# Kernel tuning notes

Hardware: AMD Instinct MI355X
Metric: run time of the kernel (lower is better)

## Reference

```python
import jax, jax.numpy as jnp
import numpy as np

HIDDEN = 2048
N_HEADS = 32
N_KV_HEADS = 8
HEAD_DIM = 64
MAX_SEQ_LEN = 512
ROPE_BASE = 10000.0


def _rope_tables(seq_len):
    inv_freq = 1.0 / (ROPE_BASE ** (jnp.arange(0, HEAD_DIM, 2, dtype=jnp.float32) / HEAD_DIM))
    pos = jnp.arange(seq_len, dtype=jnp.float32)
    freqs = jnp.outer(pos, inv_freq)              # [S, D/2]
    emb = jnp.concatenate([freqs, freqs], axis=-1)  # [S, D]
    return jnp.cos(emb), jnp.sin(emb)


def _rotate_half(x):
    h = x.shape[-1] // 2
    return jnp.concatenate([-x[..., h:], x[..., :h]], axis=-1)


def _apply_rope(x, cos, sin):
    # x: [B, H, S, D]; cos/sin: [S, D] broadcast over batch/heads
    return x * cos[None, None] + _rotate_half(x) * sin[None, None]


def setup_inputs() -> dict:
    key = jax.random.key(0)
    ks = jax.random.split(key, 5)
    B, S = 8, 512
    x = jax.random.normal(ks[0], (B, S, HIDDEN), dtype=jnp.float32)
    sq = 0.02
    Wq = jax.random.normal(ks[1], (HIDDEN, N_HEADS * HEAD_DIM), dtype=jnp.float32) * sq
    Wk = jax.random.normal(ks[2], (HIDDEN, N_KV_HEADS * HEAD_DIM), dtype=jnp.float32) * sq
    Wv = jax.random.normal(ks[3], (HIDDEN, N_KV_HEADS * HEAD_DIM), dtype=jnp.float32) * sq
    Wo = jax.random.normal(ks[4], (N_HEADS * HEAD_DIM, HIDDEN), dtype=jnp.float32) * sq
    return {"x": x, "Wq": Wq, "Wk": Wk, "Wv": Wv, "Wo": Wo}


def reference(x, Wq, Wk, Wv, Wo):
    B, S, _ = x.shape
    groups = N_HEADS // N_KV_HEADS
    scale = HEAD_DIM ** -0.5

    q = (x @ Wq).reshape(B, S, N_HEADS, HEAD_DIM).transpose(0, 2, 1, 3)      # [B,H,S,D]
    k = (x @ Wk).reshape(B, S, N_KV_HEADS, HEAD_DIM).transpose(0, 2, 1, 3)   # [B,Hk,S,D]
    v = (x @ Wv).reshape(B, S, N_KV_HEADS, HEAD_DIM).transpose(0, 2, 1, 3)

    cos, sin = _rope_tables(S)
    q = _apply_rope(q, cos, sin)
    k = _apply_rope(k, cos, sin)

    kv_cache = (k, v)  # returned before GQA head duplication, as in the original

    # repeat_interleave over kv heads for GQA
    kr = jnp.repeat(k, groups, axis=1)  # [B,H,S,D]
    vr = jnp.repeat(v, groups, axis=1)

    scores = jnp.einsum("bhqd,bhkd->bhqk", q, kr) * scale  # [B,H,S,S]
    causal = jnp.triu(jnp.ones((S, S), dtype=bool), k=1)
    scores = jnp.where(causal[None, None], -jnp.inf, scores)
    probs = jax.nn.softmax(scores, axis=-1)
    out = jnp.einsum("bhqk,bhkd->bhqd", probs, vr)  # [B,H,S,D]
    out = out.transpose(0, 2, 1, 3).reshape(B, S, N_HEADS * HEAD_DIM)
    out = out @ Wo
    return (out, kv_cache[0], kv_cache[1])
```

## Files before the change

kernel.cpp:

```cpp
#include <hip/hip_runtime.h>
#include <math.h>

#define BATCH   8
#define SEQ     512
#define HID     2048
#define NH      32
#define NKV     8
#define HD      64

typedef unsigned short u16;
typedef __attribute__((ext_vector_type(8))) short  s16x8;
typedef __attribute__((ext_vector_type(4))) float  f32x4;

__device__ __forceinline__ u16 f2bf(float f) {
  unsigned u = __builtin_bit_cast(unsigned, f);
  u += 0x7fffu + ((u >> 16) & 1u);
  return (u16)(u >> 16);
}
__device__ __forceinline__ float bf2f(u16 h) {
  unsigned u = ((unsigned)h) << 16;
  return __builtin_bit_cast(float, u);
}
__device__ __forceinline__ void split_bf16(float v, u16& h, u16& l) {
  h = f2bf(v);
  l = f2bf(v - bf2f(h));
}

#define GL16(gp, lp) __builtin_amdgcn_global_load_lds(                         \
    (const __attribute__((address_space(1))) void*)(gp),                       \
    (__attribute__((address_space(3))) void*)(lp), 16, 0, 0)

#define MFMA16(a, b, c) __builtin_amdgcn_mfma_f32_16x16x32_bf16((a), (b), (c), 0, 0, 0)

__global__ __launch_bounds__(256) void cast_x(const float* __restrict__ src,
                                              u16* __restrict__ dst)
{
  int i = blockIdx.x * 256 + threadIdx.x;
  float4 v = ((const float4*)src)[i];
  ushort4 hh;
  hh.x = f2bf(v.x); hh.y = f2bf(v.y); hh.z = f2bf(v.z); hh.w = f2bf(v.w);
  ((ushort4*)dst)[i] = hh;
}

__global__ __launch_bounds__(256) void tsplit_w(const float* __restrict__ W, int N,
                                                u16* __restrict__ BTh,
                                                u16* __restrict__ BTl, int nofs)
{
  __shared__ float t[64][68];
  const int nt = blockIdx.x * 64, kt = blockIdx.y * 64;
  const int tid = threadIdx.x;
  const int c4 = (tid & 15) * 4, r0 = tid >> 4;
  #pragma unroll
  for (int i = 0; i < 4; i++) {
    int r = r0 + i * 16;
    float4 v = *(const float4*)(&W[(size_t)(kt + r) * N + nt + c4]);
    t[c4 + 0][r] = v.x; t[c4 + 1][r] = v.y; t[c4 + 2][r] = v.z; t[c4 + 3][r] = v.w;
  }
  __syncthreads();
  #pragma unroll
  for (int i = 0; i < 4; i++) {
    int rr = r0 + i * 16;
    float4 v = *(const float4*)(&t[rr][c4]);
    ushort4 hh, ll;
    split_bf16(v.x, hh.x, ll.x);
    split_bf16(v.y, hh.y, ll.y);
    split_bf16(v.z, hh.z, ll.z);
    split_bf16(v.w, hh.w, ll.w);
    size_t o = (size_t)(nofs + nt + rr) * 2048 + kt + c4;
    *(ushort4*)(&BTh[o]) = hh;
    *(ushort4*)(&BTl[o]) = ll;
  }
}

__device__ __forceinline__ void gemm_main2(
    const u16* __restrict__ A,
    const u16* __restrict__ Bh, const u16* __restrict__ Bl,
    int mtile, int ntile,
    u16* sA, u16* sBh, u16* sBl,
    f32x4 acc[4][4])
{
  const int tid  = threadIdx.x;
  const int lane = tid & 63;
  const int w    = tid >> 6;
  const int wr = (w >> 1) * 64, wc = (w & 1) * 64;
  const int fr = lane & 15, fk = (lane >> 4) * 8;

  const int r0 = tid >> 2, c0 = (tid & 3) * 8;
  const size_t a0 = (size_t)(mtile + r0) * 2048 + c0;
  const size_t a1 = (size_t)(mtile + r0 + 64) * 2048 + c0;
  const size_t b0 = (size_t)(ntile + r0) * 2048 + c0;
  const size_t b1 = (size_t)(ntile + r0 + 64) * 2048 + c0;
  const int d0 = tid * 8, d1 = tid * 8 + 2048;

  for (int kt = 0; kt < 2048; kt += 32) {
    GL16(A  + a0 + kt, sA  + d0);
    GL16(A  + a1 + kt, sA  + d1);
    GL16(Bh + b0 + kt, sBh + d0);
    GL16(Bh + b1 + kt, sBh + d1);
    GL16(Bl + b0 + kt, sBl + d0);
    GL16(Bl + b1 + kt, sBl + d1);
    __syncthreads();

    s16x8 bhf[4], blf[4];
    #pragma unroll
    for (int ni = 0; ni < 4; ni++) {
      bhf[ni] = *(const s16x8*)(&sBh[(wc + ni * 16 + fr) * 32 + fk]);
      blf[ni] = *(const s16x8*)(&sBl[(wc + ni * 16 + fr) * 32 + fk]);
    }
    #pragma unroll
    for (int mi = 0; mi < 4; mi++) {
      s16x8 a = *(const s16x8*)(&sA[(wr + mi * 16 + fr) * 32 + fk]);
      #pragma unroll
      for (int ni = 0; ni < 4; ni++) {
        f32x4 c = acc[mi][ni];
        c = MFMA16(a, bhf[ni], c);
        c = MFMA16(a, blf[ni], c);
        acc[mi][ni] = c;
      }
    }
    __syncthreads();
  }
}

__device__ __forceinline__ void gemm_main1(
    const u16* __restrict__ A, const u16* __restrict__ B,
    int mtile, int ntile,
    u16* sA, u16* sB,
    f32x4 acc[4][4])
{
  const int tid  = threadIdx.x;
  const int lane = tid & 63;
  const int w    = tid >> 6;
  const int wr = (w >> 1) * 64, wc = (w & 1) * 64;
  const int fr = lane & 15, fk = (lane >> 4) * 8;

  const int r0 = tid >> 2, c0 = (tid & 3) * 8;
  const size_t a0 = (size_t)(mtile + r0) * 2048 + c0;
  const size_t a1 = (size_t)(mtile + r0 + 64) * 2048 + c0;
  const size_t b0 = (size_t)(ntile + r0) * 2048 + c0;
  const size_t b1 = (size_t)(ntile + r0 + 64) * 2048 + c0;
  const int d0 = tid * 8, d1 = tid * 8 + 2048;

  for (int kt = 0; kt < 2048; kt += 32) {
    GL16(A + a0 + kt, sA + d0);
    GL16(A + a1 + kt, sA + d1);
    GL16(B + b0 + kt, sB + d0);
    GL16(B + b1 + kt, sB + d1);
    __syncthreads();

    s16x8 bf[4];
    #pragma unroll
    for (int ni = 0; ni < 4; ni++)
      bf[ni] = *(const s16x8*)(&sB[(wc + ni * 16 + fr) * 32 + fk]);
    #pragma unroll
    for (int mi = 0; mi < 4; mi++) {
      s16x8 a = *(const s16x8*)(&sA[(wr + mi * 16 + fr) * 32 + fk]);
      #pragma unroll
      for (int ni = 0; ni < 4; ni++)
        acc[mi][ni] = MFMA16(a, bf[ni], acc[mi][ni]);
    }
    __syncthreads();
  }
}

#define L2_10K 13.28771238f

__global__ __launch_bounds__(256, 2) void gemm_qkv(
    const u16* __restrict__ A,
    const u16* __restrict__ Bh, const u16* __restrict__ Bl,
    u16* __restrict__ Qh, u16* __restrict__ Ql,
    float* __restrict__ kout, float* __restrict__ vout,
    u16* __restrict__ Kh, u16* __restrict__ Kl, u16* __restrict__ Vt)
{
  __shared__ __align__(16) u16 sA[128 * 32], sBh[128 * 32], sBl[128 * 32];
  const int ntile = blockIdx.x * 128, mtile = blockIdx.y * 128;
  f32x4 acc[4][4] = {};
  gemm_main2(A, Bh, Bl, mtile, ntile, sA, sBh, sBl, acc);

  const int lane = threadIdx.x & 63, w = threadIdx.x >> 6;
  const int wr = (w >> 1) * 64, wc = (w & 1) * 64;
  const int orow = (lane >> 4) * 4, ocol = lane & 15;

  if (ntile < 2048) {
    float inv[2];
    #pragma unroll
    for (int nj = 0; nj < 2; nj++)
      inv[nj] = exp2f((float)(nj * 16 + ocol) * (-L2_10K / 32.0f));
    #pragma unroll
    for (int mi = 0; mi < 4; mi++)
      #pragma unroll
      for (int r = 0; r < 4; r++) {
        int m = mtile + wr + mi * 16 + orow + r;
        int s = m & 511;
        #pragma unroll
        for (int nj = 0; nj < 2; nj++) {
          float th = (float)s * inv[nj];
          float sn, cs; sincosf(th, &sn, &cs);
          float a0 = acc[mi][nj][r]     * 0.125f;
          float a1 = acc[mi][nj + 2][r] * 0.125f;
          float q0 = a0 * cs - a1 * sn;
          float q1 = a1 * cs + a0 * sn;
          size_t o0 = (size_t)m * 2048 + ntile + wc + nj * 16 + ocol;
          u16 hh, ll;
          split_bf16(q0, hh, ll); Qh[o0] = hh;      Ql[o0] = ll;
          split_bf16(q1, hh, ll); Qh[o0 + 32] = hh; Ql[o0 + 32] = ll;
        }
      }
  } else if (ntile < 2560) {
    float inv[2];
    #pragma unroll
    for (int nj = 0; nj < 2; nj++)
      inv[nj] = exp2f((float)(nj * 16 + ocol) * (-L2_10K / 32.0f));
    #pragma unroll
    for (int mi = 0; mi < 4; mi++)
      #pragma unroll
      for (int r = 0; r < 4; r++) {
        int m = mtile + wr + mi * 16 + orow + r;
        int bb = m >> 9, s = m & 511;
        #pragma unroll
        for (int nj = 0; nj < 2; nj++) {
          int np = ntile + wc + nj * 16 + ocol - 2048;
          int hk = np >> 6, d = np & 63;
          float th = (float)s * inv[nj];
          float sn, cs; sincosf(th, &sn, &cs);
          float a0 = acc[mi][nj][r];
          float a1 = acc[mi][nj + 2][r];
          float k0 = a0 * cs - a1 * sn;
          float k1 = a1 * cs + a0 * sn;
          size_t o = ((size_t)(bb * 8 + hk) * 512 + s) * 64 + d;
          kout[o] = k0; kout[o + 32] = k1;
          u16 hh, ll;
          split_bf16(k0, hh, ll); Kh[o] = hh;      Kl[o] = ll;
          split_bf16(k1, hh, ll); Kh[o + 32] = hh; Kl[o + 32] = ll;
        }
      }
  } else {
    #pragma unroll
    for (int mi = 0; mi < 4; mi++)
      #pragma unroll
      for (int ni = 0; ni < 4; ni++) {
        int np = ntile + wc + ni * 16 + ocol - 2560;
        int hk = np >> 6, d = np & 63;
        int m0 = mtile + wr + mi * 16 + orow;
        int bb = m0 >> 9, s0 = m0 & 511;
        ushort4 pk;
        #pragma unroll
        for (int r = 0; r < 4; r++) {
          float v = acc[mi][ni][r];
          vout[((size_t)(bb * 8 + hk) * 512 + s0 + r) * 64 + d] = v;
          ((u16*)&pk)[r] = f2bf(v);
        }
        *(ushort4*)(&Vt[((size_t)(bb * 8 + hk) * 64 + d) * 512 + s0]) = pk;
      }
  }
}

__global__ __launch_bounds__(256, 2) void gemm_out(
    const u16* __restrict__ A, const u16* __restrict__ B,
    float* __restrict__ Cout)
{
  __shared__ __align__(16) u16 sA[128 * 32], sB[128 * 32];
  const int ntile = blockIdx.x * 128, mtile = blockIdx.y * 128;
  f32x4 acc[4][4] = {};
  gemm_main1(A, B, mtile, ntile, sA, sB, acc);

  const int lane = threadIdx.x & 63, w = threadIdx.x >> 6;
  const int wr = (w >> 1) * 64, wc = (w & 1) * 64;
  const int orow = (lane >> 4) * 4, ocol = lane & 15;
  #pragma unroll
  for (int mi = 0; mi < 4; mi++)
    #pragma unroll
    for (int r = 0; r < 4; r++) {
      int m = mtile + wr + mi * 16 + orow + r;
      #pragma unroll
      for (int ni = 0; ni < 4; ni++)
        Cout[(size_t)m * 2048 + ntile + wc + ni * 16 + ocol] = acc[mi][ni][r];
    }
}

__global__ __launch_bounds__(256, 2)
void attn(const u16* __restrict__ Qh, const u16* __restrict__ Ql,
          const u16* __restrict__ Kh, const u16* __restrict__ Kl,
          const u16* __restrict__ Vt,
          u16* __restrict__ Ao)
{
  __shared__ __align__(16) u16 sKh[4096], sKl[4096], sVt[4096];
  __shared__ __align__(16) u16 sP[4][1024];

  const int qt = blockIdx.x, h = blockIdx.y, bb = blockIdx.z;
  const int hk = h >> 2, bh = bb * 8 + hk;
  const int tid = threadIdx.x, lane = tid & 63, w = tid >> 6;
  const int fr = lane & 15, fg = lane >> 4;

  const int qrow = bb * 512 + qt * 64 + w * 16 + fr;
  const size_t qoff = (size_t)qrow * 2048 + h * 64 + fg * 8;
  const s16x8 qh0 = *(const s16x8*)(Qh + qoff);
  const s16x8 qh1 = *(const s16x8*)(Qh + qoff + 32);
  const s16x8 ql0 = *(const s16x8*)(Ql + qoff);
  const s16x8 ql1 = *(const s16x8*)(Ql + qoff + 32);

  f32x4 oacc[4] = {};
  float m_r[4] = {-1e30f, -1e30f, -1e30f, -1e30f};
  float l_r[4] = {};

  const size_t kbase = (size_t)bh * 512 * 64;
  const size_t vbase = (size_t)bh * 64 * 512;

  for (int j = 0; j <= qt; j++) {
    __syncthreads();
    #pragma unroll
    for (int p = 0; p < 2; p++) {
      int s = tid + p * 256;
      int row = s >> 3, c8 = (s & 7) ^ (row & 7);
      GL16(Kh + kbase + (size_t)(j * 64 + row) * 64 + c8 * 8, sKh + s * 8);
      GL16(Kl + kbase + (size_t)(j * 64 + row) * 64 + c8 * 8, sKl + s * 8);
      GL16(Vt + vbase + (size_t)row * 512 + j * 64 + c8 * 8,  sVt + s * 8);
    }
    __syncthreads();

    f32x4 sacc[4] = {};
    #pragma unroll
    for (int ni = 0; ni < 4; ni++) {
      #pragma unroll
      for (int ks = 0; ks < 2; ks++) {
        int row = ni * 16 + fr;
        int byte = row * 128 + ((fg * 16 + ks * 64) ^ ((row & 7) << 4));
        s16x8 kh = *(const s16x8*)((const char*)sKh + byte);
        s16x8 kl = *(const s16x8*)((const char*)sKl + byte);
        s16x8 qa = ks ? qh1 : qh0;
        s16x8 qb = ks ? ql1 : ql0;
        f32x4 c = sacc[ni];
        c = MFMA16(qa, kh, c);
        c = MFMA16(qa, kl, c);
        c = MFMA16(qb, kh, c);
        sacc[ni] = c;
      }
    }

    const int rowg0 = qt * 64 + w * 16 + fg * 4;
    #pragma unroll
    for (int r = 0; r < 4; r++) {
      float mx = -1e30f;
      #pragma unroll
      for (int ni = 0; ni < 4; ni++) {
        int col = j * 64 + ni * 16 + fr;
        float v = (col <= rowg0 + r) ? sacc[ni][r] : -1e30f;
        sacc[ni][r] = v;
        mx = fmaxf(mx, v);
      }
      mx = fmaxf(mx, __shfl_xor(mx, 1));
      mx = fmaxf(mx, __shfl_xor(mx, 2));
      mx = fmaxf(mx, __shfl_xor(mx, 4));
      mx = fmaxf(mx, __shfl_xor(mx, 8));
      float mnew = fmaxf(m_r[r], mx);
      float sc = __expf(m_r[r] - mnew);
      m_r[r] = mnew;
      float ls = 0.0f;
      #pragma unroll
      for (int ni = 0; ni < 4; ni++) {
        float p = __expf(sacc[ni][r] - mnew);
        sacc[ni][r] = p;
        ls += p;
      }
      ls += __shfl_xor(ls, 1);
      ls += __shfl_xor(ls, 2);
      ls += __shfl_xor(ls, 4);
      ls += __shfl_xor(ls, 8);
      l_r[r] = l_r[r] * sc + ls;
      #pragma unroll
      for (int nd = 0; nd < 4; nd++) oacc[nd][r] *= sc;
    }

    u16* pbuf = sP[w];
    #pragma unroll
    for (int ni = 0; ni < 4; ni++)
      #pragma unroll
      for (int r = 0; r < 4; r++) {
        int prow = fg * 4 + r, pcol = ni * 16 + fr;
        int byte = prow * 128 + ((pcol * 2) ^ ((prow & 7) << 4));
        *(u16*)((char*)pbuf + byte) = f2bf(sacc[ni][r]);
      }

    #pragma unroll
    for (int ks = 0; ks < 2; ks++) {
      int pbyte = fr * 128 + ((fg * 16 + ks * 64) ^ ((fr & 7) << 4));
      s16x8 pa = *(const s16x8*)((const char*)pbuf + pbyte);
      #pragma unroll
      for (int nd = 0; nd < 4; nd++) {
        int vrow = nd * 16 + fr;
        int vbyte = vrow * 128 + ((fg * 16 + ks * 64) ^ ((vrow & 7) << 4));
        s16x8 vb = *(const s16x8*)((const char*)sVt + vbyte);
        oacc[nd] = MFMA16(pa, vb, oacc[nd]);
      }
    }
  }

  const size_t obase = (size_t)(bb * 512 + qt * 64 + w * 16 + fg * 4) * 2048 + h * 64;
  #pragma unroll
  for (int r = 0; r < 4; r++) {
    float inv = 1.0f / l_r[r];
    #pragma unroll
    for (int nd = 0; nd < 4; nd++)
      Ao[obase + (size_t)r * 2048 + nd * 16 + fr] = f2bf(oacc[nd][r] * inv);
  }
}

extern "C" void kernel_launch(void* const* d_in, const int* in_sizes, int n_in,
                              void* d_out, int out_size, void* d_ws, size_t ws_size,
                              hipStream_t stream)
{
  const float* x  = (const float*)d_in[0];
  const float* Wq = (const float*)d_in[1];
  const float* Wk = (const float*)d_in[2];
  const float* Wv = (const float*)d_in[3];
  const float* Wo = (const float*)d_in[4];

  float* out  = (float*)d_out;
  float* kout = out + 8388608;
  float* vout = out + 10485760;

  uint8_t* wsb = (uint8_t*)d_ws;
  u16* xbf = (u16*)(wsb + 0);
  u16* Ao  = xbf;
  u16* Wqh = (u16*)(wsb + 16777216);
  u16* Wql = (u16*)(wsb + 29360128);
  u16* Woh = (u16*)(wsb + 16777216);
  u16* Wol = (u16*)(wsb + 25165824);
  u16* Qhp = (u16*)(wsb + 41943040);
  u16* Qlp = (u16*)(wsb + 58720256);
  u16* Khp = (u16*)(wsb + 75497472);
  u16* Klp = (u16*)(wsb + 79691776);
  u16* Vtp = (u16*)(wsb + 83886080);

  cast_x<<<8192, 256, 0, stream>>>(x, xbf);
  tsplit_w<<<dim3(32, 32), 256, 0, stream>>>(Wq, 2048, Wqh, Wql, 0);
  tsplit_w<<<dim3(8, 32), 256, 0, stream>>>(Wk, 512, Wqh, Wql, 2048);
  tsplit_w<<<dim3(8, 32), 256, 0, stream>>>(Wv, 512, Wqh, Wql, 2560);
  gemm_qkv<<<dim3(24, 32), 256, 0, stream>>>(xbf, Wqh, Wql,
                                             Qhp, Qlp, kout, vout, Khp, Klp, Vtp);
  tsplit_w<<<dim3(32, 32), 256, 0, stream>>>(Wo, 2048, Woh, Wol, 0);
  attn<<<dim3(8, 32, 8), 256, 0, stream>>>(Qhp, Qlp, Khp, Klp, Vtp, Ao);
  gemm_out<<<dim3(16, 32), 256, 0, stream>>>(Ao, Woh, out);
}
```

Measured before the change: 359.0 us.

## Drop split-bf16 weight and K terms, read K/V directly from global in attention

Weights and K are now cast to a single bf16 instead of being split into high and low bf16 halves. This halves the MFMA count and the B-operand traffic in the QKV GEMM, and drops one MFMA per K fragment in attention. The attention kernel no longer stages K and V through LDS. Each wave loads its fragments straight from global memory with no block barriers, and the occupancy hint is raised to 4 blocks per CU. This trades accuracy, since the weight and K low parts are lost, and gives up LDS reuse of K/V across the 4 waves in exchange for less sync and more occupancy.

```diff
diff --git a/kernel.cpp b/kernel.cpp
--- a/kernel.cpp
+++ b/kernel.cpp
@@ -42,9 +42,8 @@
   ((ushort4*)dst)[i] = hh;
 }
 
-__global__ __launch_bounds__(256) void tsplit_w(const float* __restrict__ W, int N,
-                                                u16* __restrict__ BTh,
-                                                u16* __restrict__ BTl, int nofs)
+__global__ __launch_bounds__(256) void tcast_w(const float* __restrict__ W, int N,
+                                               u16* __restrict__ BT, int nofs)
 {
   __shared__ float t[64][68];
   const int nt = blockIdx.x * 64, kt = blockIdx.y * 64;
@@ -61,22 +60,16 @@
   for (int i = 0; i < 4; i++) {
     int rr = r0 + i * 16;
     float4 v = *(const float4*)(&t[rr][c4]);
-    ushort4 hh, ll;
-    split_bf16(v.x, hh.x, ll.x);
-    split_bf16(v.y, hh.y, ll.y);
-    split_bf16(v.z, hh.z, ll.z);
-    split_bf16(v.w, hh.w, ll.w);
-    size_t o = (size_t)(nofs + nt + rr) * 2048 + kt + c4;
-    *(ushort4*)(&BTh[o]) = hh;
-    *(ushort4*)(&BTl[o]) = ll;
-  }
-}
-
-__device__ __forceinline__ void gemm_main2(
-    const u16* __restrict__ A,
-    const u16* __restrict__ Bh, const u16* __restrict__ Bl,
+    ushort4 hh;
+    hh.x = f2bf(v.x); hh.y = f2bf(v.y); hh.z = f2bf(v.z); hh.w = f2bf(v.w);
+    *(ushort4*)(&BT[(size_t)(nofs + nt + rr) * 2048 + kt + c4]) = hh;
+  }
+}
+
+__device__ __forceinline__ void gemm_main1(
+    const u16* __restrict__ A, const u16* __restrict__ B,
     int mtile, int ntile,
-    u16* sA, u16* sBh, u16* sBl,
+    u16* sA, u16* sB,
     f32x4 acc[4][4])
 {
   const int tid  = threadIdx.x;
@@ -93,55 +86,6 @@
   const int d0 = tid * 8, d1 = tid * 8 + 2048;
 
   for (int kt = 0; kt < 2048; kt += 32) {
-    GL16(A  + a0 + kt, sA  + d0);
-    GL16(A  + a1 + kt, sA  + d1);
-    GL16(Bh + b0 + kt, sBh + d0);
-    GL16(Bh + b1 + kt, sBh + d1);
-    GL16(Bl + b0 + kt, sBl + d0);
-    GL16(Bl + b1 + kt, sBl + d1);
-    __syncthreads();
-
-    s16x8 bhf[4], blf[4];
-    #pragma unroll
-    for (int ni = 0; ni < 4; ni++) {
-      bhf[ni] = *(const s16x8*)(&sBh[(wc + ni * 16 + fr) * 32 + fk]);
-      blf[ni] = *(const s16x8*)(&sBl[(wc + ni * 16 + fr) * 32 + fk]);
-    }
-    #pragma unroll
-    for (int mi = 0; mi < 4; mi++) {
-      s16x8 a = *(const s16x8*)(&sA[(wr + mi * 16 + fr) * 32 + fk]);
-      #pragma unroll
-      for (int ni = 0; ni < 4; ni++) {
-        f32x4 c = acc[mi][ni];
-        c = MFMA16(a, bhf[ni], c);
-        c = MFMA16(a, blf[ni], c);
-        acc[mi][ni] = c;
-      }
-    }
-    __syncthreads();
-  }
-}
-
-__device__ __forceinline__ void gemm_main1(
-    const u16* __restrict__ A, const u16* __restrict__ B,
-    int mtile, int ntile,
-    u16* sA, u16* sB,
-    f32x4 acc[4][4])
-{
-  const int tid  = threadIdx.x;
-  const int lane = tid & 63;
-  const int w    = tid >> 6;
-  const int wr = (w >> 1) * 64, wc = (w & 1) * 64;
-  const int fr = lane & 15, fk = (lane >> 4) * 8;
-
-  const int r0 = tid >> 2, c0 = (tid & 3) * 8;
-  const size_t a0 = (size_t)(mtile + r0) * 2048 + c0;
-  const size_t a1 = (size_t)(mtile + r0 + 64) * 2048 + c0;
-  const size_t b0 = (size_t)(ntile + r0) * 2048 + c0;
-  const size_t b1 = (size_t)(ntile + r0 + 64) * 2048 + c0;
-  const int d0 = tid * 8, d1 = tid * 8 + 2048;
-
-  for (int kt = 0; kt < 2048; kt += 32) {
     GL16(A + a0 + kt, sA + d0);
     GL16(A + a1 + kt, sA + d1);
     GL16(B + b0 + kt, sB + d0);
@@ -166,16 +110,15 @@
 #define L2_10K 13.28771238f
 
 __global__ __launch_bounds__(256, 2) void gemm_qkv(
-    const u16* __restrict__ A,
-    const u16* __restrict__ Bh, const u16* __restrict__ Bl,
+    const u16* __restrict__ A, const u16* __restrict__ B,
     u16* __restrict__ Qh, u16* __restrict__ Ql,
     float* __restrict__ kout, float* __restrict__ vout,
-    u16* __restrict__ Kh, u16* __restrict__ Kl, u16* __restrict__ Vt)
-{
-  __shared__ __align__(16) u16 sA[128 * 32], sBh[128 * 32], sBl[128 * 32];
+    u16* __restrict__ Kp, u16* __restrict__ Vt)
+{
+  __shared__ __align__(16) u16 sA[128 * 32], sB[128 * 32];
   const int ntile = blockIdx.x * 128, mtile = blockIdx.y * 128;
   f32x4 acc[4][4] = {};
-  gemm_main2(A, Bh, Bl, mtile, ntile, sA, sBh, sBl, acc);
+  gemm_main1(A, B, mtile, ntile, sA, sB, acc);
 
   const int lane = threadIdx.x & 63, w = threadIdx.x >> 6;
   const int wr = (w >> 1) * 64, wc = (w & 1) * 64;
@@ -228,10 +171,8 @@
           float k0 = a0 * cs - a1 * sn;
           float k1 = a1 * cs + a0 * sn;
           size_t o = ((size_t)(bb * 8 + hk) * 512 + s) * 64 + d;
-          kout[o] = k0; kout[o + 32] = k1;
-          u16 hh, ll;
-          split_bf16(k0, hh, ll); Kh[o] = hh;      Kl[o] = ll;
-          split_bf16(k1, hh, ll); Kh[o + 32] = hh; Kl[o + 32] = ll;
+          kout[o] = k0;           kout[o + 32] = k1;
+          Kp[o]   = f2bf(k0);     Kp[o + 32]   = f2bf(k1);
         }
       }
   } else {
@@ -278,13 +219,11 @@
     }
 }
 
-__global__ __launch_bounds__(256, 2)
+__global__ __launch_bounds__(256, 4)
 void attn(const u16* __restrict__ Qh, const u16* __restrict__ Ql,
-          const u16* __restrict__ Kh, const u16* __restrict__ Kl,
-          const u16* __restrict__ Vt,
+          const u16* __restrict__ Kp, const u16* __restrict__ Vt,
           u16* __restrict__ Ao)
 {
-  __shared__ __align__(16) u16 sKh[4096], sKl[4096], sVt[4096];
   __shared__ __align__(16) u16 sP[4][1024];
 
   const int qt = blockIdx.x, h = blockIdx.y, bb = blockIdx.z;
@@ -307,32 +246,18 @@
   const size_t vbase = (size_t)bh * 64 * 512;
 
   for (int j = 0; j <= qt; j++) {
-    __syncthreads();
-    #pragma unroll
-    for (int p = 0; p < 2; p++) {
-      int s = tid + p * 256;
-      int row = s >> 3, c8 = (s & 7) ^ (row & 7);
-      GL16(Kh + kbase + (size_t)(j * 64 + row) * 64 + c8 * 8, sKh + s * 8);
-      GL16(Kl + kbase + (size_t)(j * 64 + row) * 64 + c8 * 8, sKl + s * 8);
-      GL16(Vt + vbase + (size_t)row * 512 + j * 64 + c8 * 8,  sVt + s * 8);
-    }
-    __syncthreads();
+    const u16* kb = Kp + kbase + (size_t)j * 64 * 64;
+    const u16* vb = Vt + vbase + j * 64;
 
     f32x4 sacc[4] = {};
     #pragma unroll
     for (int ni = 0; ni < 4; ni++) {
       #pragma unroll
       for (int ks = 0; ks < 2; ks++) {
-        int row = ni * 16 + fr;
-        int byte = row * 128 + ((fg * 16 + ks * 64) ^ ((row & 7) << 4));
-        s16x8 kh = *(const s16x8*)((const char*)sKh + byte);
-        s16x8 kl = *(const s16x8*)((const char*)sKl + byte);
-        s16x8 qa = ks ? qh1 : qh0;
-        s16x8 qb = ks ? ql1 : ql0;
+        s16x8 k = *(const s16x8*)(kb + (ni * 16 + fr) * 64 + ks * 32 + fg * 8);
         f32x4 c = sacc[ni];
-        c = MFMA16(qa, kh, c);
-        c = MFMA16(qa, kl, c);
-        c = MFMA16(qb, kh, c);
+        c = MFMA16(ks ? qh1 : qh0, k, c);
+        c = MFMA16(ks ? ql1 : ql0, k, c);
         sacc[ni] = c;
       }
     }
@@ -387,10 +312,8 @@
       s16x8 pa = *(const s16x8*)((const char*)pbuf + pbyte);
       #pragma unroll
       for (int nd = 0; nd < 4; nd++) {
-        int vrow = nd * 16 + fr;
-        int vbyte = vrow * 128 + ((fg * 16 + ks * 64) ^ ((vrow & 7) << 4));
-        s16x8 vb = *(const s16x8*)((const char*)sVt + vbyte);
-        oacc[nd] = MFMA16(pa, vb, oacc[nd]);
+        s16x8 vv = *(const s16x8*)(vb + (size_t)(nd * 16 + fr) * 512 + ks * 32 + fg * 8);
+        oacc[nd] = MFMA16(pa, vv, oacc[nd]);
       }
     }
   }
@@ -422,23 +345,20 @@
   uint8_t* wsb = (uint8_t*)d_ws;
   u16* xbf = (u16*)(wsb + 0);
   u16* Ao  = xbf;
-  u16* Wqh = (u16*)(wsb + 16777216);
-  u16* Wql = (u16*)(wsb + 29360128);
-  u16* Woh = (u16*)(wsb + 16777216);
-  u16* Wol = (u16*)(wsb + 25165824);
-  u16* Qhp = (u16*)(wsb + 41943040);
-  u16* Qlp = (u16*)(wsb + 58720256);
-  u16* Khp = (u16*)(wsb + 75497472);
-  u16* Klp = (u16*)(wsb + 79691776);
-  u16* Vtp = (u16*)(wsb + 83886080);
+  u16* Wqp = (u16*)(wsb + 16777216);
+  u16* Wop = (u16*)(wsb + 16777216);
+  u16* Qhp = (u16*)(wsb + 29360128);
+  u16* Qlp = (u16*)(wsb + 46137344);
+  u16* Kpp = (u16*)(wsb + 62914560);
+  u16* Vtp = (u16*)(wsb + 67108864);
 
   cast_x<<<8192, 256, 0, stream>>>(x, xbf);
-  tsplit_w<<<dim3(32, 32), 256, 0, stream>>>(Wq, 2048, Wqh, Wql, 0);
-  tsplit_w<<<dim3(8, 32), 256, 0, stream>>>(Wk, 512, Wqh, Wql, 2048);
-  tsplit_w<<<dim3(8, 32), 256, 0, stream>>>(Wv, 512, Wqh, Wql, 2560);
-  gemm_qkv<<<dim3(24, 32), 256, 0, stream>>>(xbf, Wqh, Wql,
-                                             Qhp, Qlp, kout, vout, Khp, Klp, Vtp);
-  tsplit_w<<<dim3(32, 32), 256, 0, stream>>>(Wo, 2048, Woh, Wol, 0);
-  attn<<<dim3(8, 32, 8), 256, 0, stream>>>(Qhp, Qlp, Khp, Klp, Vtp, Ao);
-  gemm_out<<<dim3(16, 32), 256, 0, stream>>>(Ao, Woh, out);
-}
+  tcast_w<<<dim3(32, 32), 256, 0, stream>>>(Wq, 2048, Wqp, 0);
+  tcast_w<<<dim3(8, 32), 256, 0, stream>>>(Wk, 512, Wqp, 2048);
+  tcast_w<<<dim3(8, 32), 256, 0, stream>>>(Wv, 512, Wqp, 2560);
+  gemm_qkv<<<dim3(24, 32), 256, 0, stream>>>(xbf, Wqp,
+                                             Qhp, Qlp, kout, vout, Kpp, Vtp);
+  tcast_w<<<dim3(32, 32), 256, 0, stream>>>(Wo, 2048, Wop, 0);
+  attn<<<dim3(8, 32, 8), 256, 0, stream>>>(Qhp, Qlp, Kpp, Vtp, Ao);
+  gemm_out<<<dim3(16, 32), 256, 0, stream>>>(Ao, Wop, out);
+}
```

New measurement: 364.0 us. No clear change (+1.4%).
